# Kernel tuning notes

Hardware: AMD Instinct MI355X
Metric: run time of the kernel (lower is better)

## Reference

```python
import jax, jax.numpy as jnp
import numpy as np

INPUT_SIZE = 784
HIDDEN_SIZE = 256
NUM_CLASSES = 10
BATCH = 32768


def setup_inputs() -> dict:
    key = jax.random.key(0)
    k_x, k_w1, k_b1, k_w2, k_b2 = jax.random.split(key, 5)
    return {
        "x": jax.random.normal(k_x, (BATCH, INPUT_SIZE), dtype=jnp.float32),
        "fc1_weight": jax.random.normal(k_w1, (HIDDEN_SIZE, INPUT_SIZE), dtype=jnp.float32),
        "fc1_bias": jax.random.normal(k_b1, (HIDDEN_SIZE,), dtype=jnp.float32),
        "fc2_weight": jax.random.normal(k_w2, (NUM_CLASSES, HIDDEN_SIZE), dtype=jnp.float32),
        "fc2_bias": jax.random.normal(k_b2, (NUM_CLASSES,), dtype=jnp.float32),
    }


def reference(x, fc1_weight, fc1_bias, fc2_weight, fc2_bias):
    # hidden = x @ W1^T + b1, ReLU
    hidden = jnp.einsum("bi,hi->bh", x, fc1_weight) + fc1_bias
    activated = jnp.maximum(hidden, 0.0)
    # output = activated @ W2^T + b2
    logits = jnp.einsum("bh,ch->bc", activated, fc2_weight) + fc2_bias
    return jax.nn.softmax(logits, axis=-1)
```

## Files before the change

### kernel.cpp

```cpp
#include <hip/hip_runtime.h>
#include <math.h>

#define BATCH_N   32768
#define IN_F      784
#define HID_F     256
#define NCLS      10
#define BM        64
#define NTHREADS  512
#define NRND      13

typedef __attribute__((ext_vector_type(8))) short short8;
typedef __attribute__((ext_vector_type(4))) float f32x4;

#define WS_W1H 0
#define WS_W1L 409600

union S8U { short8 s; uint4 u; };

__device__ __forceinline__ void cvt8(float4 a, float4 b, short8* hi, short8* lo) {
    const unsigned M = 0xFFFF0000u;
    const unsigned ux = __float_as_uint(a.x), uy = __float_as_uint(a.y),
                   uz = __float_as_uint(a.z), uw = __float_as_uint(a.w),
                   vx = __float_as_uint(b.x), vy = __float_as_uint(b.y),
                   vz = __float_as_uint(b.z), vw = __float_as_uint(b.w);
    S8U h, l;
    h.u.x = (ux >> 16) | (uy & M);
    h.u.y = (uz >> 16) | (uw & M);
    h.u.z = (vx >> 16) | (vy & M);
    h.u.w = (vz >> 16) | (vw & M);
    const float rx = a.x - __uint_as_float(ux & M);
    const float ry = a.y - __uint_as_float(uy & M);
    const float rz = a.z - __uint_as_float(uz & M);
    const float rw = a.w - __uint_as_float(uw & M);
    const float sx = b.x - __uint_as_float(vx & M);
    const float sy = b.y - __uint_as_float(vy & M);
    const float sz = b.z - __uint_as_float(vz & M);
    const float sw_ = b.w - __uint_as_float(vw & M);
    l.u.x = (__float_as_uint(rx) >> 16) | (__float_as_uint(ry) & M);
    l.u.y = (__float_as_uint(rz) >> 16) | (__float_as_uint(rw) & M);
    l.u.z = (__float_as_uint(sx) >> 16) | (__float_as_uint(sy) & M);
    l.u.w = (__float_as_uint(sz) >> 16) | (__float_as_uint(sw_) & M);
    *hi = h.s; *lo = l.s;
}

__global__ __launch_bounds__(256)
void prep_w1_kernel(const float* __restrict__ w1, char* __restrict__ ws) {
    const int s    = blockIdx.x * 256 + threadIdx.x;
    const int lane = s & 63, ct = (s >> 6) & 15, kt = s >> 10;
    const int n    = ct * 16 + (lane & 15);
    const int k0   = kt * 32 + (lane >> 4) * 8;
    float4 a = make_float4(0.f, 0.f, 0.f, 0.f), b = a;
    if (k0 + 7 < IN_F) {
        const float* p = w1 + (size_t)n * IN_F + k0;
        a = *(const float4*)p;
        b = *(const float4*)(p + 4);
    }
    short8 hi, lo;
    cvt8(a, b, &hi, &lo);
    *(short8*)(ws + WS_W1H + (size_t)s * 16) = hi;
    *(short8*)(ws + WS_W1L + (size_t)s * 16) = lo;
}

__global__ __launch_bounds__(NTHREADS, 4)
void mlp_mfma_kernel(const float* __restrict__ x,
                     const char*  __restrict__ wsb,
                     const float* __restrict__ b1,
                     const float* __restrict__ w2,
                     const float* __restrict__ b2,
                     float* __restrict__ out)
{
    __shared__ short8 xh[2][512];
    __shared__ short8 xl[2][512];
    __shared__ float  hid[64 * 128];

    const int tid  = threadIdx.x;
    const int lane = tid & 63;
    const int wv   = tid >> 6;
    const int wc   = wv & 3;
    const int wr   = wv >> 2;
    const int m    = lane & 15;
    const int quad = lane >> 4;
    const int row0 = blockIdx.x * BM;

    const int slr = tid >> 3;
    const int sks = tid & 7;
    const float* xs = x + (size_t)(row0 + slr) * IN_F + sks * 8;
    const int swidx = slr * 8 + (sks ^ (slr & 7));

    const int rb  = (wr * 32 + m) * 8;
    const int sl0 = rb + (quad ^ (m & 7));
    const int sl1 = rb + ((4 + quad) ^ (m & 7));

    const char* bhp = wsb + WS_W1H + ((size_t)(wc * 4) * 64 + lane) * 16;
    const char* blp = wsb + WS_W1L + ((size_t)(wc * 4) * 64 + lane) * 16;

    f32x4 acc[2][4];
    #pragma unroll
    for (int a = 0; a < 2; ++a)
        #pragma unroll
        for (int b = 0; b < 4; ++b)
            acc[a][b] = (f32x4){0.f, 0.f, 0.f, 0.f};

    {
        float4 a = *(const float4*)(xs);
        float4 b = *(const float4*)(xs + 4);
        short8 hi, lo;
        cvt8(a, b, &hi, &lo);
        xh[0][swidx] = hi;
        xl[0][swidx] = lo;
    }
    __syncthreads();

    int cur = 0;
    for (int r = 0; r < NRND - 1; ++r) {
        const int kn = (r + 1) * 64 + sks * 8;
        float4 xa = make_float4(0.f, 0.f, 0.f, 0.f), xb = xa;
        if (kn + 7 < IN_F) {
            xa = *(const float4*)(xs + (r + 1) * 64);
            xb = *(const float4*)(xs + (r + 1) * 64 + 4);
        }
        #pragma unroll
        for (int kk = 0; kk < 2; ++kk) {
            const int kt = r * 2 + kk;
            short8 bh[4], bl[4];
            #pragma unroll
            for (int c = 0; c < 4; ++c) {
                bh[c] = *(const short8*)(bhp + (size_t)kt * 16384 + c * 1024);
                bl[c] = *(const short8*)(blp + (size_t)kt * 16384 + c * 1024);
            }
            const int sl = kk ? sl1 : sl0;
            short8 ah[2], al[2];
            #pragma unroll
            for (int rt = 0; rt < 2; ++rt) {
                ah[rt] = xh[cur][sl + rt * 128];
                al[rt] = xl[cur][sl + rt * 128];
            }
            #pragma unroll
            for (int rt = 0; rt < 2; ++rt)
                #pragma unroll
                for (int c = 0; c < 4; ++c) {
                    acc[rt][c] = __builtin_amdgcn_mfma_f32_16x16x32_bf16(ah[rt], bh[c], acc[rt][c], 0, 0, 0);
                    acc[rt][c] = __builtin_amdgcn_mfma_f32_16x16x32_bf16(al[rt], bh[c], acc[rt][c], 0, 0, 0);
                    acc[rt][c] = __builtin_amdgcn_mfma_f32_16x16x32_bf16(ah[rt], bl[c], acc[rt][c], 0, 0, 0);
                }
        }
        {
            short8 hi, lo;
            cvt8(xa, xb, &hi, &lo);
            xh[cur ^ 1][swidx] = hi;
            xl[cur ^ 1][swidx] = lo;
        }
        __syncthreads();
        cur ^= 1;
    }

    {
        const int kt = 24;
        short8 bh[4], bl[4];
        #pragma unroll
        for (int c = 0; c < 4; ++c) {
            bh[c] = *(const short8*)(bhp + (size_t)kt * 16384 + c * 1024);
            bl[c] = *(const short8*)(blp + (size_t)kt * 16384 + c * 1024);
        }
        short8 ah[2], al[2];
        #pragma unroll
        for (int rt = 0; rt < 2; ++rt) {
            ah[rt] = xh[cur][sl0 + rt * 128];
            al[rt] = xl[cur][sl0 + rt * 128];
        }
        #pragma unroll
        for (int rt = 0; rt < 2; ++rt)
            #pragma unroll
            for (int c = 0; c < 4; ++c) {
                acc[rt][c] = __builtin_amdgcn_mfma_f32_16x16x32_bf16(ah[rt], bh[c], acc[rt][c], 0, 0, 0);
                acc[rt][c] = __builtin_amdgcn_mfma_f32_16x16x32_bf16(al[rt], bh[c], acc[rt][c], 0, 0, 0);
                acc[rt][c] = __builtin_amdgcn_mfma_f32_16x16x32_bf16(ah[rt], bl[c], acc[rt][c], 0, 0, 0);
            }
    }

    const int rl    = tid >> 3;
    const int slice = tid & 7;
    const int gb    = (slice >> 1) * 64 + (slice & 1) * 16;
    const int cb    = slice * 16;
    const int sw2   = (rl & 7) << 2;

    float lg[NCLS];
    #pragma unroll
    for (int k = 0; k < NCLS; ++k) lg[k] = 0.f;

    #pragma unroll
    for (int p = 0; p < 2; ++p) {
        __syncthreads();
        #pragma unroll
        for (int cl = 0; cl < 2; ++cl) {
            const int c  = 2 * p + cl;
            const int g  = (wc * 4 + c) * 16 + m;
            const float bv = b1[g];
            const int cc = wc * 32 + cl * 16 + m;
            #pragma unroll
            for (int rt = 0; rt < 2; ++rt)
                #pragma unroll
                for (int reg = 0; reg < 4; ++reg) {
                    const int row = wr * 32 + rt * 16 + quad * 4 + reg;
                    hid[row * 128 + (cc ^ ((row & 7) << 2))] =
                        fmaxf(acc[rt][c][reg] + bv, 0.f);
                }
        }
        __syncthreads();
        #pragma unroll
        for (int i = 0; i < 4; ++i) {
            const float4 h = *(const float4*)(hid + rl * 128 + ((cb + i * 4) ^ sw2));
            const int g4 = gb + 32 * p + i * 4;
            #pragma unroll
            for (int k = 0; k < NCLS; ++k) {
                const float4 w = *(const float4*)(w2 + k * HID_F + g4);
                lg[k] += h.x * w.x + h.y * w.y + h.z * w.z + h.w * w.w;
            }
        }
    }

    #pragma unroll
    for (int k = 0; k < NCLS; ++k) {
        float v = lg[k];
        v += __shfl_xor(v, 1);
        v += __shfl_xor(v, 2);
        v += __shfl_xor(v, 4);
        lg[k] = v + b2[k];
    }
    float mx = -1e30f;
    #pragma unroll
    for (int k = 0; k < NCLS; ++k) mx = fmaxf(mx, lg[k]);
    float s = 0.f;
    #pragma unroll
    for (int k = 0; k < NCLS; ++k) { lg[k] = __expf(lg[k] - mx); s += lg[k]; }
    const float inv = 1.f / s;
    float* o = out + (size_t)(row0 + rl) * NCLS;
    o[slice] = lg[slice] * inv;
    if (slice < 2) o[8 + slice] = lg[8 + slice] * inv;
}

extern "C" void kernel_launch(void* const* d_in, const int* in_sizes, int n_in,
                              void* d_out, int out_size, void* d_ws, size_t ws_size,
                              hipStream_t stream)
{
    const float* x  = (const float*)d_in[0];
    const float* w1 = (const float*)d_in[1];
    const float* b1 = (const float*)d_in[2];
    const float* w2 = (const float*)d_in[3];
    const float* b2 = (const float*)d_in[4];
    float* out = (float*)d_out;

    hipLaunchKernelGGL(prep_w1_kernel, dim3(100), dim3(256), 0, stream,
                       w1, (char*)d_ws);
    hipLaunchKernelGGL(mlp_mfma_kernel, dim3(BATCH_N / BM), dim3(NTHREADS), 0, stream,
                       x, (const char*)d_ws, b1, w2, b2, out);
}
```

Baseline: 206.2 us.

## Double the K stage depth, software-prefetch W1 fragments, and union LDS buffers

Each pipeline stage now covers 128 K elements instead of 64, so there are half as many block barriers per row tile. W1 bf16 fragments are loaded one k-tile ahead into registers so the global loads overlap the MFMAs. The x staging buffers and the hidden buffer share one LDS union, which keeps LDS use flat despite the larger stage, and s_setprio raises wave priority around the MFMA bursts. Output writes use a select tree instead of dynamic register indexing. The trade-off is more registers for the prefetched fragments and the wider x loads, which may reduce occupancy.

```diff
diff --git a/kernel.cpp b/kernel.cpp
--- a/kernel.cpp
+++ b/kernel.cpp
@@ -7,7 +7,6 @@
 #define NCLS      10
 #define BM        64
 #define NTHREADS  512
-#define NRND      13
 
 typedef __attribute__((ext_vector_type(8))) short short8;
 typedef __attribute__((ext_vector_type(4))) float f32x4;
@@ -69,9 +68,10 @@
                      const float* __restrict__ b2,
                      float* __restrict__ out)
 {
-    __shared__ short8 xh[2][512];
-    __shared__ short8 xl[2][512];
-    __shared__ float  hid[64 * 128];
+    __shared__ union {
+        struct { short8 xh[2][1024]; short8 xl[2][1024]; } st;
+        float hid[64 * 128];
+    } sm;
 
     const int tid  = threadIdx.x;
     const int lane = tid & 63;
@@ -82,14 +82,15 @@
     const int quad = lane >> 4;
     const int row0 = blockIdx.x * BM;
 
-    const int slr = tid >> 3;
-    const int sks = tid & 7;
-    const float* xs = x + (size_t)(row0 + slr) * IN_F + sks * 8;
-    const int swidx = slr * 8 + (sks ^ (slr & 7));
-
-    const int rb  = (wr * 32 + m) * 8;
-    const int sl0 = rb + (quad ^ (m & 7));
-    const int sl1 = rb + ((4 + quad) ^ (m & 7));
+    const int slr  = tid >> 3;
+    const int ks16 = tid & 7;
+    const float* xs = x + (size_t)(row0 + slr) * IN_F + ks16 * 16;
+    const int wb0 = slr * 16 + (((ks16 * 2)    ) ^ (slr & 7));
+    const int wb1 = slr * 16 + (((ks16 * 2) + 1) ^ (slr & 7));
+
+    const int msw = m & 7;
+    const int rb0 = (wr * 32 + m) * 16;
+    const int rb1 = rb0 + 256;
 
     const char* bhp = wsb + WS_W1H + ((size_t)(wc * 4) * 64 + lane) * 16;
     const char* blp = wsb + WS_W1L + ((size_t)(wc * 4) * 64 + lane) * 16;
@@ -101,81 +102,94 @@
         for (int b = 0; b < 4; ++b)
             acc[a][b] = (f32x4){0.f, 0.f, 0.f, 0.f};
 
+    short8 bhc[4], blc[4];
+    #pragma unroll
+    for (int c = 0; c < 4; ++c) {
+        bhc[c] = *(const short8*)(bhp + c * 1024);
+        blc[c] = *(const short8*)(blp + c * 1024);
+    }
     {
-        float4 a = *(const float4*)(xs);
-        float4 b = *(const float4*)(xs + 4);
-        short8 hi, lo;
-        cvt8(a, b, &hi, &lo);
-        xh[0][swidx] = hi;
-        xl[0][swidx] = lo;
+        const float4 a0 = *(const float4*)(xs);
+        const float4 a1 = *(const float4*)(xs + 4);
+        const float4 a2 = *(const float4*)(xs + 8);
+        const float4 a3 = *(const float4*)(xs + 12);
+        short8 h0, l0, h1, l1;
+        cvt8(a0, a1, &h0, &l0);
+        cvt8(a2, a3, &h1, &l1);
+        sm.st.xh[0][wb0] = h0; sm.st.xl[0][wb0] = l0;
+        sm.st.xh[0][wb1] = h1; sm.st.xl[0][wb1] = l1;
     }
     __syncthreads();
 
     int cur = 0;
-    for (int r = 0; r < NRND - 1; ++r) {
-        const int kn = (r + 1) * 64 + sks * 8;
-        float4 xa = make_float4(0.f, 0.f, 0.f, 0.f), xb = xa;
-        if (kn + 7 < IN_F) {
-            xa = *(const float4*)(xs + (r + 1) * 64);
-            xb = *(const float4*)(xs + (r + 1) * 64 + 4);
-        }
-        #pragma unroll
-        for (int kk = 0; kk < 2; ++kk) {
-            const int kt = r * 2 + kk;
-            short8 bh[4], bl[4];
+    for (int r = 0; r < 6; ++r) {
+        const short8* xhr = sm.st.xh[cur];
+        const short8* xlr = sm.st.xl[cur];
+        const int k0n = (r + 1) * 128 + ks16 * 16;
+        float4 xa0 = make_float4(0.f, 0.f, 0.f, 0.f), xa1 = xa0, xa2 = xa0, xa3 = xa0;
+        if (k0n < IN_F) {
+            const float* p = xs + (r + 1) * 128;
+            xa0 = *(const float4*)(p);
+            xa1 = *(const float4*)(p + 4);
+            xa2 = *(const float4*)(p + 8);
+            xa3 = *(const float4*)(p + 12);
+        }
+        #pragma unroll
+        for (int ktl = 0; ktl < 4; ++ktl) {
+            const int kt = r * 4 + ktl;
+            short8 bhn[4], bln[4];
             #pragma unroll
             for (int c = 0; c < 4; ++c) {
-                bh[c] = *(const short8*)(bhp + (size_t)kt * 16384 + c * 1024);
-                bl[c] = *(const short8*)(blp + (size_t)kt * 16384 + c * 1024);
-            }
-            const int sl = kk ? sl1 : sl0;
-            short8 ah[2], al[2];
+                bhn[c] = *(const short8*)(bhp + (size_t)(kt + 1) * 16384 + c * 1024);
+                bln[c] = *(const short8*)(blp + (size_t)(kt + 1) * 16384 + c * 1024);
+            }
+            __builtin_amdgcn_s_setprio(1);
             #pragma unroll
             for (int rt = 0; rt < 2; ++rt) {
-                ah[rt] = xh[cur][sl + rt * 128];
-                al[rt] = xl[cur][sl + rt * 128];
-            }
-            #pragma unroll
-            for (int rt = 0; rt < 2; ++rt)
+                const int sl = (rt ? rb1 : rb0) + ((ktl * 4 + quad) ^ msw);
+                const short8 ah = xhr[sl];
+                const short8 al = xlr[sl];
                 #pragma unroll
                 for (int c = 0; c < 4; ++c) {
-                    acc[rt][c] = __builtin_amdgcn_mfma_f32_16x16x32_bf16(ah[rt], bh[c], acc[rt][c], 0, 0, 0);
-                    acc[rt][c] = __builtin_amdgcn_mfma_f32_16x16x32_bf16(al[rt], bh[c], acc[rt][c], 0, 0, 0);
-                    acc[rt][c] = __builtin_amdgcn_mfma_f32_16x16x32_bf16(ah[rt], bl[c], acc[rt][c], 0, 0, 0);
+                    acc[rt][c] = __builtin_amdgcn_mfma_f32_16x16x32_bf16(ah, bhc[c], acc[rt][c], 0, 0, 0);
+                    acc[rt][c] = __builtin_amdgcn_mfma_f32_16x16x32_bf16(al, bhc[c], acc[rt][c], 0, 0, 0);
+                    acc[rt][c] = __builtin_amdgcn_mfma_f32_16x16x32_bf16(ah, blc[c], acc[rt][c], 0, 0, 0);
                 }
+            }
+            __builtin_amdgcn_s_setprio(0);
+            #pragma unroll
+            for (int c = 0; c < 4; ++c) { bhc[c] = bhn[c]; blc[c] = bln[c]; }
         }
         {
-            short8 hi, lo;
-            cvt8(xa, xb, &hi, &lo);
-            xh[cur ^ 1][swidx] = hi;
-            xl[cur ^ 1][swidx] = lo;
+            short8 h0, l0, h1, l1;
+            cvt8(xa0, xa1, &h0, &l0);
+            cvt8(xa2, xa3, &h1, &l1);
+            short8* xhw = sm.st.xh[cur ^ 1];
+            short8* xlw = sm.st.xl[cur ^ 1];
+            xhw[wb0] = h0; xlw[wb0] = l0;
+            xhw[wb1] = h1; xlw[wb1] = l1;
         }
         __syncthreads();
         cur ^= 1;
     }
 
     {
-        const int kt = 24;
-        short8 bh[4], bl[4];
-        #pragma unroll
-        for (int c = 0; c < 4; ++c) {
-            bh[c] = *(const short8*)(bhp + (size_t)kt * 16384 + c * 1024);
-            bl[c] = *(const short8*)(blp + (size_t)kt * 16384 + c * 1024);
-        }
-        short8 ah[2], al[2];
+        const short8* xhr = sm.st.xh[cur];
+        const short8* xlr = sm.st.xl[cur];
+        __builtin_amdgcn_s_setprio(1);
         #pragma unroll
         for (int rt = 0; rt < 2; ++rt) {
-            ah[rt] = xh[cur][sl0 + rt * 128];
-            al[rt] = xl[cur][sl0 + rt * 128];
-        }
-        #pragma unroll
-        for (int rt = 0; rt < 2; ++rt)
+            const int sl = (rt ? rb1 : rb0) + (quad ^ msw);
+            const short8 ah = xhr[sl];
+            const short8 al = xlr[sl];
             #pragma unroll
             for (int c = 0; c < 4; ++c) {
-                acc[rt][c] = __builtin_amdgcn_mfma_f32_16x16x32_bf16(ah[rt], bh[c], acc[rt][c], 0, 0, 0);
-                acc[rt][c] = __builtin_amdgcn_mfma_f32_16x16x32_bf16(al[rt], bh[c], acc[rt][c], 0, 0, 0);
-                acc[rt][c] = __builtin_amdgcn_mfma_f32_16x16x32_bf16(ah[rt], bl[c], acc[rt][c], 0, 0, 0);
-            }
+                acc[rt][c] = __builtin_amdgcn_mfma_f32_16x16x32_bf16(ah, bhc[c], acc[rt][c], 0, 0, 0);
+                acc[rt][c] = __builtin_amdgcn_mfma_f32_16x16x32_bf16(al, bhc[c], acc[rt][c], 0, 0, 0);
+                acc[rt][c] = __builtin_amdgcn_mfma_f32_16x16x32_bf16(ah, blc[c], acc[rt][c], 0, 0, 0);
+            }
+        }
+        __builtin_amdgcn_s_setprio(0);
     }
 
     const int rl    = tid >> 3;
@@ -202,14 +216,14 @@
                 #pragma unroll
                 for (int reg = 0; reg < 4; ++reg) {
                     const int row = wr * 32 + rt * 16 + quad * 4 + reg;
-                    hid[row * 128 + (cc ^ ((row & 7) << 2))] =
+                    sm.hid[row * 128 + (cc ^ ((row & 7) << 2))] =
                         fmaxf(acc[rt][c][reg] + bv, 0.f);
                 }
         }
         __syncthreads();
         #pragma unroll
         for (int i = 0; i < 4; ++i) {
-            const float4 h = *(const float4*)(hid + rl * 128 + ((cb + i * 4) ^ sw2));
+            const float4 h = *(const float4*)(sm.hid + rl * 128 + ((cb + i * 4) ^ sw2));
             const int g4 = gb + 32 * p + i * 4;
             #pragma unroll
             for (int k = 0; k < NCLS; ++k) {
@@ -234,9 +248,13 @@
     #pragma unroll
     for (int k = 0; k < NCLS; ++k) { lg[k] = __expf(lg[k] - mx); s += lg[k]; }
     const float inv = 1.f / s;
+    const float va = (slice & 4)
+        ? ((slice & 2) ? ((slice & 1) ? lg[7] : lg[6]) : ((slice & 1) ? lg[5] : lg[4]))
+        : ((slice & 2) ? ((slice & 1) ? lg[3] : lg[2]) : ((slice & 1) ? lg[1] : lg[0]));
+    const float vb = (slice & 1) ? lg[9] : lg[8];
     float* o = out + (size_t)(row0 + rl) * NCLS;
-    o[slice] = lg[slice] * inv;
-    if (slice < 2) o[8 + slice] = lg[8 + slice] * inv;
+    o[slice] = va * inv;
+    if (slice < 2) o[8 + slice] = vb * inv;
 }
 
 extern "C" void kernel_launch(void* const* d_in, const int* in_sizes, int n_in,
```

Result: slower. 225.2 us (+9.2%).
